# Optimization experiments

Measured on AMD Instinct MI355X. Metric: run time of the kernel, lower is better.

## Reference

```python
import jax, jax.numpy as jnp
import numpy as np

V, F, H, R = 10000, 768, 768, 49
B, T = 128, 32


def setup_inputs() -> dict:
    key = jax.random.key(0)
    ks = jax.random.split(key, 12)
    s = lambda *sh: 1.0 / np.sqrt(sh[-1])
    return {
        "features": jax.random.normal(ks[0], (B, R, F), jnp.float32),
        "captions": jax.random.randint(ks[1], (B, T), 0, V),
        "emb_W": jax.random.normal(ks[2], (V, H), jnp.float32),
        "attn_W": jax.random.normal(ks[3], (H, F + H), jnp.float32) * s(H, F + H),
        "attn_b": jnp.zeros((H,), jnp.float32),
        "attnv_W": jax.random.normal(ks[4], (1, H), jnp.float32) * s(1, H),
        "attnv_b": jnp.zeros((1,), jnp.float32),
        "W_ih": jax.random.normal(ks[5], (4 * H, H + F), jnp.float32) * s(1, H),
        "W_hh": jax.random.normal(ks[6], (4 * H, H), jnp.float32) * s(1, H),
        "b_ih": jnp.zeros((4 * H,), jnp.float32),
        "b_hh": jnp.zeros((4 * H,), jnp.float32),
        "fc_W": jax.random.normal(ks[7], (V, H), jnp.float32) * s(V, H),
        "fc_b": jnp.zeros((V,), jnp.float32),
    }


def reference(features, captions, emb_W, attn_W, attn_b, attnv_W, attnv_b,
              W_ih, W_hh, b_ih, b_hh, fc_W, fc_b):
    # initial hidden state (hidden_state=None branch)
    h0 = jnp.tanh(features.mean(axis=1))           # [B,H]
    c0 = jnp.zeros_like(h0)                        # [B,H]
    emb = emb_W[captions]                          # [B,T,H]

    # split attn_linear weight into feature/hidden parts; feature projection is
    # time-invariant so compute once outside the scan.
    Wf, Wh = attn_W[:, :F], attn_W[:, F:]
    feat_proj = jnp.einsum('brf,hf->brh', features, Wf)   # [B,R,H]
    v = attnv_W[0]                                 # [H]
    bias = b_ih + b_hh                             # [4H]

    def step(carry, emb_t):
        h, c = carry
        attn_hidden = jnp.tanh(feat_proj + (h @ Wh.T)[:, None, :] + attn_b)  # [B,R,H]
        scores = attn_hidden @ v + attnv_b[0]      # [B,R]
        alpha = jax.nn.softmax(scores, axis=1)
        context = jnp.einsum('br,brf->bf', alpha, features)  # [B,F]
        x = jnp.concatenate([emb_t, context], axis=1)        # [B,H+F]
        gates = x @ W_ih.T + h @ W_hh.T + bias     # [B,4H]
        i, f, g, o = jnp.split(gates, 4, axis=1)
        c_new = jax.nn.sigmoid(f) * c + jax.nn.sigmoid(i) * jnp.tanh(g)
        h_new = jax.nn.sigmoid(o) * jnp.tanh(c_new)
        out_t = h_new @ fc_W.T + fc_b              # [B,V] (dropout = identity, eval)
        return (h_new, c_new), out_t

    (h, c), outs = jax.lax.scan(step, (h0, c0), jnp.swapaxes(emb, 0, 1))
    outputs = jnp.swapaxes(outs, 0, 1)             # [B,T,V]
    return outputs, (h, c)
```

## Files before the change

### kernel.cpp

```cpp
#include <hip/hip_runtime.h>


typedef _Float16 f16x8 __attribute__((ext_vector_type(8)));
typedef _Float16 f16x4 __attribute__((ext_vector_type(4)));
typedef float f32x4 __attribute__((ext_vector_type(4)));

#define NB 128
#define NT 32
#define NV 10000
#define NH 768
#define NR 49
#define OUT_ELEMS 40960000

__device__ __forceinline__ float fast_tanh(float x) {
  x = fminf(9.f, fmaxf(-9.f, x));
  float e = __expf(2.f * x);
  return (e - 1.f) / (e + 1.f);
}
__device__ __forceinline__ float sigm(float x) { return 1.f / (1.f + __expf(-x)); }

__device__ __forceinline__ void gld16(const void* g, void* l) {
  __builtin_amdgcn_global_load_lds((const __attribute__((address_space(1))) void*)g,
                                   (__attribute__((address_space(3))) void*)l, 16, 0, 0);
}

template <int BM, int BN, int EPI>
__global__ __launch_bounds__(256) void gemm_f16(
    const _Float16* __restrict__ A, int lda,
    const _Float16* __restrict__ Bt, int ldb,
    void* __restrict__ Cv, const float* __restrict__ bias,
    int M, int N, int ksteps, int ksplit) {
  constexpr int BK = 64;
  __shared__ __attribute__((aligned(16))) _Float16 sAB[(BM + BN) * BK];
  _Float16* sA = sAB;
  _Float16* sB = sAB + BM * BK;
  const int tid = threadIdx.x;
  const int m0 = blockIdx.x * BM, n0 = blockIdx.y * BN;
  const int z = blockIdx.z;
  A += (size_t)z * ksplit;
  Bt += (size_t)z * ksplit;

  constexpr int WM = BM / 2, WN = BN / 2;
  constexpr int MF = WM / 16, NF = WN / 16;
  const int wid = tid >> 6, lane = tid & 63;
  const int wr = wid >> 1, wc = wid & 1;
  const int lr = lane & 15;
  const int lk = (lane >> 4) * 8;

  f32x4 acc[MF][NF] = {};

  for (int kt = 0; kt < ksteps; ++kt) {
    const int kbase = kt * BK;
#pragma unroll
    for (int i = 0; i < BM / 32; i++) {
      int idx = tid + i * 256;
      int row = idx >> 3, seg = idx & 7;
      gld16(A + (size_t)(m0 + row) * lda + kbase + seg * 8, sA + idx * 8);
    }
#pragma unroll
    for (int i = 0; i < BN / 32; i++) {
      int idx = tid + i * 256;
      int row = idx >> 3, seg = idx & 7;
      gld16(Bt + (size_t)(n0 + row) * ldb + kbase + seg * 8, sB + idx * 8);
    }
    __syncthreads();
#pragma unroll
    for (int kk = 0; kk < 2; ++kk) {
      f16x8 af[MF], bf[NF];
#pragma unroll
      for (int m = 0; m < MF; m++)
        af[m] = *(const f16x8*)&sA[(wr * WM + m * 16 + lr) * BK + kk * 32 + lk];
#pragma unroll
      for (int n = 0; n < NF; n++)
        bf[n] = *(const f16x8*)&sB[(wc * WN + n * 16 + lr) * BK + kk * 32 + lk];
#pragma unroll
      for (int m = 0; m < MF; m++)
#pragma unroll
        for (int n = 0; n < NF; n++)
          acc[m][n] = __builtin_amdgcn_mfma_f32_16x16x32_f16(af[m], bf[n], acc[m][n], 0, 0, 0);
    }
    __syncthreads();
  }

  const int rowb = (lane >> 4) * 4;
#pragma unroll
  for (int m = 0; m < MF; m++) {
    int gm = m0 + wr * WM + m * 16 + rowb;
#pragma unroll
    for (int n = 0; n < NF; n++) {
      int gn = n0 + wc * WN + n * 16 + lr;
#pragma unroll
      for (int j = 0; j < 4; j++) {
        int r = gm + j;
        if (EPI == 1) {
          float* C = (float*)Cv + (size_t)z * M * N;
          C[(size_t)r * N + gn] = acc[m][n][j];
        } else if (EPI == 3) {
          ((_Float16*)Cv)[(size_t)r * N + gn] = (_Float16)(acc[m][n][j] + bias[gn]);
        } else {
          ((_Float16*)Cv)[(size_t)r * N + gn] = (_Float16)acc[m][n][j];
        }
      }
    }
  }
}

__global__ __launch_bounds__(512) void gemm_fc(
    const _Float16* __restrict__ A, const _Float16* __restrict__ Bt,
    float* __restrict__ out, const float* __restrict__ bias, int N) {
  constexpr int BK = 64;
  __shared__ __attribute__((aligned(16))) _Float16 sAB[256 * BK];
  _Float16* sA = sAB;
  _Float16* sB = sAB + 128 * BK;
  const int tid = threadIdx.x;
  const int m0 = blockIdx.x * 128, n0 = blockIdx.y * 128;
  const int wid = tid >> 6, lane = tid & 63;
  const int wr = wid >> 1;
  const int wc = wid & 1;
  const int lr = lane & 15;
  const int lk = (lane >> 4) * 8;

  f32x4 acc[2][4] = {};

  for (int kt = 0; kt < 12; ++kt) {
    const int kbase = kt * BK;
#pragma unroll
    for (int i = 0; i < 2; i++) {
      int idx = tid + i * 512;
      int row = idx >> 3, seg = idx & 7;
      gld16(A + (size_t)(m0 + row) * NH + kbase + seg * 8, sA + idx * 8);
      int gr = n0 + row;
      if (gr >= N) gr = N - 1;
      gld16(Bt + (size_t)gr * NH + kbase + seg * 8, sB + idx * 8);
    }
    __syncthreads();
#pragma unroll
    for (int kk = 0; kk < 2; ++kk) {
      f16x8 af[2], bf[4];
#pragma unroll
      for (int m = 0; m < 2; m++)
        af[m] = *(const f16x8*)&sA[(wr * 32 + m * 16 + lr) * BK + kk * 32 + lk];
#pragma unroll
      for (int n = 0; n < 4; n++)
        bf[n] = *(const f16x8*)&sB[(wc * 64 + n * 16 + lr) * BK + kk * 32 + lk];
#pragma unroll
      for (int m = 0; m < 2; m++)
#pragma unroll
        for (int n = 0; n < 4; n++)
          acc[m][n] = __builtin_amdgcn_mfma_f32_16x16x32_f16(af[m], bf[n], acc[m][n], 0, 0, 0);
    }
    __syncthreads();
  }

  const int rowb = (lane >> 4) * 4;
  float* sC = (float*)sAB;
#pragma unroll
  for (int h = 0; h < 2; h++) {
    if ((wr >> 1) == h) {
#pragma unroll
      for (int m = 0; m < 2; m++)
#pragma unroll
        for (int n = 0; n < 4; n++)
#pragma unroll
          for (int j = 0; j < 4; j++)
            sC[((wr & 1) * 32 + m * 16 + rowb + j) * 128 + wc * 64 + n * 16 + lr] =
                acc[m][n][j];
    }
    __syncthreads();
#pragma unroll
    for (int i = 0; i < 4; i++) {
      int lrow = (tid >> 5) + i * 16;
      int col = (tid & 31) * 4;
      int gn = n0 + col;
      if (gn < N) {
        int r = m0 + h * 64 + lrow;
        int tt = r >> 7, b = r & 127;
        f32x4 val = *(f32x4*)&sC[lrow * 128 + col];
        f32x4 bb = *(const f32x4*)&bias[gn];
        val += bb;
        *(f32x4*)&out[((size_t)(b * NT + tt)) * NV + gn] = val;
      }
    }
    __syncthreads();
  }
}

__global__ __launch_bounds__(256) void k_scores(
    const _Float16* __restrict__ fp, const float* __restrict__ g1,
    const float* __restrict__ v, float* __restrict__ sc) {
  int wid = threadIdx.x >> 6, lane = threadIdx.x & 63;
  int p = blockIdx.x * 4 + wid;
  int b = p / NR;
  const _Float16* fpr = fp + (size_t)p * NH;
  const float* hw0 = g1 + (size_t)b * 3840;
  const float* hw1 = g1 + (size_t)NB * 3840 + (size_t)b * 3840;
  float s = 0.f;
#pragma unroll
  for (int it = 0; it < 3; it++) {
    int h = it * 256 + lane * 4;
    f16x4 fv = *(const f16x4*)(fpr + h);
    f32x4 a0 = *(const f32x4*)(hw0 + h);
    f32x4 a1 = *(const f32x4*)(hw1 + h);
    f32x4 vv = *(const f32x4*)(v + h);
#pragma unroll
    for (int j = 0; j < 4; j++) s += fast_tanh((float)fv[j] + a0[j] + a1[j]) * vv[j];
  }
#pragma unroll
  for (int off = 32; off; off >>= 1) s += __shfl_down(s, off);
  if (lane == 0) sc[p] = s;
}

__global__ __launch_bounds__(256) void k_ctx(const float* __restrict__ sc,
                                             const _Float16* __restrict__ feat16,
                                             _Float16* __restrict__ ctx16) {
  __shared__ float al[64];
  int b = blockIdx.x, tid = threadIdx.x;
  if (tid < 64) {
    float s = (tid < NR) ? sc[b * NR + tid] : -1e30f;
    float m = s;
#pragma unroll
    for (int off = 32; off; off >>= 1) m = fmaxf(m, __shfl_xor(m, off));
    float e = (tid < NR) ? __expf(s - m) : 0.f;
    float su = e;
#pragma unroll
    for (int off = 32; off; off >>= 1) su += __shfl_xor(su, off);
    al[tid] = e / su;
  }
  __syncthreads();
  int f = blockIdx.y * 256 + tid;
  const _Float16* fb = feat16 + (size_t)b * NR * NH + f;
  float acc = 0.f;
#pragma unroll
  for (int r = 0; r < NR; r++) acc += al[r] * (float)fb[(size_t)r * NH];
  ctx16[(size_t)b * NH + f] = (_Float16)acc;
}

__global__ void k_lstm2(const _Float16* __restrict__ ge_t, const float* __restrict__ g1,
                        const float* __restrict__ g2, const float* __restrict__ b_ih,
                        const float* __restrict__ b_hh, float* __restrict__ h,
                        float* __restrict__ c, _Float16* __restrict__ h16,
                        _Float16* __restrict__ Hall_t) {
  int b = blockIdx.x;
  int hh = blockIdx.y * 256 + threadIdx.x;
  const _Float16* ge = ge_t + (size_t)b * 3072;
  const float* a0 = g1 + (size_t)b * 3840 + 768;
  const float* a1 = g1 + (size_t)NB * 3840 + (size_t)b * 3840 + 768;
  const float* c0 = g2 + (size_t)b * 3072;
  const float* c1 = g2 + (size_t)NB * 3072 + (size_t)b * 3072;
  float gi = (float)ge[hh] + a0[hh] + a1[hh] + c0[hh] + c1[hh] + b_ih[hh] + b_hh[hh];
  float gf = (float)ge[768 + hh] + a0[768 + hh] + a1[768 + hh] + c0[768 + hh] + c1[768 + hh] +
             b_ih[768 + hh] + b_hh[768 + hh];
  float gg = (float)ge[1536 + hh] + a0[1536 + hh] + a1[1536 + hh] + c0[1536 + hh] +
             c1[1536 + hh] + b_ih[1536 + hh] + b_hh[1536 + hh];
  float go = (float)ge[2304 + hh] + a0[2304 + hh] + a1[2304 + hh] + c0[2304 + hh] +
             c1[2304 + hh] + b_ih[2304 + hh] + b_hh[2304 + hh];
  float i_ = sigm(gi), f_ = sigm(gf), g_ = fast_tanh(gg), o_ = sigm(go);
  float cn = f_ * c[b * NH + hh] + i_ * g_;
  float hn = o_ * fast_tanh(cn);
  c[b * NH + hh] = cn;
  h[b * NH + hh] = hn;
  h16[(size_t)b * NH + hh] = (_Float16)hn;
  Hall_t[(size_t)b * NH + hh] = (_Float16)hn;
}

__global__ void k_prep(const float* __restrict__ features, const float* __restrict__ attn_W,
                       const float* __restrict__ W_ih, const float* __restrict__ W_hh,
                       const int* __restrict__ captions, const float* __restrict__ emb_W,
                       _Float16* __restrict__ feat16, _Float16* __restrict__ Wf16,
                       _Float16* __restrict__ W1, _Float16* __restrict__ We,
                       _Float16* __restrict__ Wc, _Float16* __restrict__ emb16,
                       float* __restrict__ h, float* __restrict__ c,
                       _Float16* __restrict__ h16) {
  const int blk = blockIdx.x, tid = threadIdx.x;
  if (blk < 18816) {
    int i = blk * 256 + tid;
    feat16[i] = (_Float16)features[i];
  } else if (blk < 21120) {
    int q = (blk - 18816) * 256 + tid;
    int j = q / NH, k = q - j * NH;
    Wf16[q] = (_Float16)attn_W[(size_t)j * 1536 + k];
  } else if (blk < 32640) {
    int q = (blk - 21120) * 256 + tid;
    int j = q / NH, k = q - j * NH;
    W1[q] = (_Float16)(j < NH ? attn_W[(size_t)j * 1536 + 768 + k]
                              : W_hh[(size_t)(j - NH) * NH + k]);
  } else if (blk < 41856) {
    int q = (blk - 32640) * 256 + tid;
    int j = q / NH, k = q - j * NH;
    We[q] = (_Float16)W_ih[(size_t)j * 1536 + k];
  } else if (blk < 51072) {
    int q = (blk - 41856) * 256 + tid;
    int j = q / NH, k = q - j * NH;
    Wc[q] = (_Float16)W_ih[(size_t)j * 1536 + 768 + k];
  } else if (blk < 63360) {
    int q = (blk - 51072) * 256 + tid;
    int row = q / NH, k = q - row * NH;
    int t = row >> 7, b = row & 127;
    int tok = captions[b * NT + t];
    emb16[q] = (_Float16)emb_W[(size_t)tok * NH + k];
  } else {
    int q = blk - 63360;
    int b = q / 3;
    int f = (q - b * 3) * 256 + tid;
    float s = 0.f;
#pragma unroll 7
    for (int r = 0; r < NR; r++) s += features[((size_t)(b * NR + r)) * NH + f];
    float h0 = tanhf(s * (1.f / 49.f));
    h[b * NH + f] = h0;
    c[b * NH + f] = 0.f;
    h16[(size_t)b * NH + f] = (_Float16)h0;
  }
}

__global__ void k_f32_to_f16(const float* __restrict__ src, _Float16* __restrict__ dst, int n) {
  int i = blockIdx.x * 256 + threadIdx.x;
  if (i < n) dst[i] = (_Float16)src[i];
}

__global__ void k_tail(const float* __restrict__ h, const float* __restrict__ c,
                       float* __restrict__ out) {
  int i = blockIdx.x * 256 + threadIdx.x;
  out[OUT_ELEMS + i] = h[i];
  out[OUT_ELEMS + NB * NH + i] = c[i];
}

extern "C" void kernel_launch(void* const* d_in, const int* in_sizes, int n_in,
                              void* d_out, int out_size, void* d_ws, size_t ws_size,
                              hipStream_t stream) {
  const float* features = (const float*)d_in[0];
  const int* captions = (const int*)d_in[1];
  const float* emb_W = (const float*)d_in[2];
  const float* attn_W = (const float*)d_in[3];
  const float* attn_b = (const float*)d_in[4];
  const float* attnv_W = (const float*)d_in[5];
  const float* W_ih = (const float*)d_in[7];
  const float* W_hh = (const float*)d_in[8];
  const float* b_ih = (const float*)d_in[9];
  const float* b_hh = (const float*)d_in[10];
  const float* fc_W = (const float*)d_in[11];
  const float* fc_b = (const float*)d_in[12];
  float* out = (float*)d_out;

  char* p = (char*)d_ws;
  _Float16* Gemb16 = (_Float16*)p;  p += 25165824;
  _Float16* fcW16 = Gemb16;
  _Float16* emb16 = (_Float16*)p;   p += 6291456;
  _Float16* feat16 = (_Float16*)p;  p += 9633792;
  _Float16* fp16 = (_Float16*)p;    p += 9633792;
  _Float16* Wf16 = (_Float16*)p;    p += 1179648;
  _Float16* W1 = (_Float16*)p;      p += 5898240;
  _Float16* We16 = (_Float16*)p;    p += 4718592;
  _Float16* Wc16 = (_Float16*)p;    p += 4718592;
  _Float16* H_all = (_Float16*)p;   p += 6291456;
  float* g1 = (float*)p;            p += 3932160;
  float* g2 = (float*)p;            p += 3145728;
  float* scores = (float*)p;        p += 25088;
  _Float16* ctx16 = (_Float16*)p;   p += 196608;
  _Float16* h16 = (_Float16*)p;     p += 196608;
  float* hbuf = (float*)p;          p += 393216;
  float* cbuf = (float*)p;          p += 393216;

  k_prep<<<dim3(63744), 256, 0, stream>>>(features, attn_W, W_ih, W_hh, captions, emb_W,
                                          feat16, Wf16, W1, We16, Wc16, emb16,
                                          hbuf, cbuf, h16);
  gemm_f16<128, 128, 3><<<dim3(49, 6, 1), 256, 0, stream>>>(
      feat16, 768, Wf16, 768, fp16, attn_b, 6272, 768, 12, 0);
  gemm_f16<128, 128, 4><<<dim3(32, 24, 1), 256, 0, stream>>>(
      emb16, 768, We16, 768, Gemb16, nullptr, 4096, 3072, 12, 0);

  for (int t = 0; t < NT; t++) {
    if (t > 0)
      k_lstm2<<<dim3(128, 3), 256, 0, stream>>>(
          Gemb16 + (size_t)(t - 1) * NB * 3072, g1, g2, b_ih, b_hh, hbuf, cbuf, h16,
          H_all + (size_t)(t - 1) * NB * NH);
    gemm_f16<64, 64, 1><<<dim3(2, 60, 2), 256, 0, stream>>>(
        h16, 768, W1, 768, g1, nullptr, 128, 3840, 6, 384);
    k_scores<<<dim3(1568), 256, 0, stream>>>(fp16, g1, attnv_W, scores);
    k_ctx<<<dim3(128, 3), 256, 0, stream>>>(scores, feat16, ctx16);
    gemm_f16<64, 64, 1><<<dim3(2, 48, 2), 256, 0, stream>>>(
        ctx16, 768, Wc16, 768, g2, nullptr, 128, 3072, 6, 384);
  }
  k_lstm2<<<dim3(128, 3), 256, 0, stream>>>(
      Gemb16 + (size_t)(NT - 1) * NB * 3072, g1, g2, b_ih, b_hh, hbuf, cbuf, h16,
      H_all + (size_t)(NT - 1) * NB * NH);

  k_f32_to_f16<<<dim3(30000), 256, 0, stream>>>(fc_W, fcW16, 7680000);
  gemm_fc<<<dim3(32, 79), 512, 0, stream>>>(H_all, fcW16, out, fc_b, NV);
  k_tail<<<dim3(384), 256, 0, stream>>>(hbuf, cbuf, out);
}
```

Baseline: 1.111 ms.

## Shrink critical-path GEMM per step and move W_hh product off it

The per-step hidden projection GEMM now covers only the attention part (Wh, 768 columns) with a 3-way K split, so k_scores waits on a smaller GEMM. The W_hh gate product moves into the context GEMM launch as extra z-slices (4-way partial buffers), and k_lstm2 sums four partials. The two setup GEMMs are merged into one launch, and gemm_fc switches to 256 threads with larger per-warp tiles. The trade-off is more partial-sum traffic in lstm and fewer waves in gemm_fc.

```diff
diff --git a/kernel.cpp b/kernel.cpp
--- a/kernel.cpp
+++ b/kernel.cpp
@@ -24,59 +24,114 @@
                                    (__attribute__((address_space(3))) void*)l, 16, 0, 0);
 }
 
-template <int BM, int BN, int EPI>
-__global__ __launch_bounds__(256) void gemm_f16(
-    const _Float16* __restrict__ A, int lda,
-    const _Float16* __restrict__ Bt, int ldb,
-    void* __restrict__ Cv, const float* __restrict__ bias,
-    int M, int N, int ksteps, int ksplit) {
+template <int KSTEPS, int KSPLIT>
+__global__ __launch_bounds__(256) void gemm64(
+    const _Float16* __restrict__ A, const _Float16* __restrict__ Bt,
+    float* __restrict__ C, int N) {
   constexpr int BK = 64;
-  __shared__ __attribute__((aligned(16))) _Float16 sAB[(BM + BN) * BK];
+  __shared__ __attribute__((aligned(16))) _Float16 sAB[128 * BK];
   _Float16* sA = sAB;
-  _Float16* sB = sAB + BM * BK;
+  _Float16* sB = sAB + 64 * BK;
   const int tid = threadIdx.x;
-  const int m0 = blockIdx.x * BM, n0 = blockIdx.y * BN;
+  const int m0 = blockIdx.x * 64, n0 = blockIdx.y * 64;
   const int z = blockIdx.z;
-  A += (size_t)z * ksplit;
-  Bt += (size_t)z * ksplit;
-
-  constexpr int WM = BM / 2, WN = BN / 2;
-  constexpr int MF = WM / 16, NF = WN / 16;
+  A += (size_t)z * KSPLIT;
+  Bt += (size_t)z * KSPLIT;
+  C += (size_t)z * 128 * N;
+
   const int wid = tid >> 6, lane = tid & 63;
   const int wr = wid >> 1, wc = wid & 1;
-  const int lr = lane & 15;
-  const int lk = (lane >> 4) * 8;
-
-  f32x4 acc[MF][NF] = {};
-
-  for (int kt = 0; kt < ksteps; ++kt) {
+  const int lr = lane & 15, lk = (lane >> 4) * 8;
+
+  f32x4 acc[2][2] = {};
+
+  for (int kt = 0; kt < KSTEPS; ++kt) {
     const int kbase = kt * BK;
 #pragma unroll
-    for (int i = 0; i < BM / 32; i++) {
+    for (int i = 0; i < 2; i++) {
       int idx = tid + i * 256;
       int row = idx >> 3, seg = idx & 7;
-      gld16(A + (size_t)(m0 + row) * lda + kbase + seg * 8, sA + idx * 8);
-    }
-#pragma unroll
-    for (int i = 0; i < BN / 32; i++) {
+      gld16(A + (size_t)(m0 + row) * NH + kbase + seg * 8, sA + idx * 8);
+      gld16(Bt + (size_t)(n0 + row) * NH + kbase + seg * 8, sB + idx * 8);
+    }
+    __syncthreads();
+#pragma unroll
+    for (int kk = 0; kk < 2; ++kk) {
+      f16x8 af[2], bf[2];
+#pragma unroll
+      for (int m = 0; m < 2; m++)
+        af[m] = *(const f16x8*)&sA[(wr * 32 + m * 16 + lr) * BK + kk * 32 + lk];
+#pragma unroll
+      for (int n = 0; n < 2; n++)
+        bf[n] = *(const f16x8*)&sB[(wc * 32 + n * 16 + lr) * BK + kk * 32 + lk];
+#pragma unroll
+      for (int m = 0; m < 2; m++)
+#pragma unroll
+        for (int n = 0; n < 2; n++)
+          acc[m][n] = __builtin_amdgcn_mfma_f32_16x16x32_f16(af[m], bf[n], acc[m][n], 0, 0, 0);
+    }
+    __syncthreads();
+  }
+
+  const int rowb = (lane >> 4) * 4;
+#pragma unroll
+  for (int m = 0; m < 2; m++) {
+    int gm = m0 + wr * 32 + m * 16 + rowb;
+#pragma unroll
+    for (int n = 0; n < 2; n++) {
+      int gn = n0 + wc * 32 + n * 16 + lr;
+#pragma unroll
+      for (int j = 0; j < 4; j++) C[(size_t)(gm + j) * N + gn] = acc[m][n][j];
+    }
+  }
+}
+
+__global__ __launch_bounds__(256) void gemm_g2m(
+    const _Float16* __restrict__ ctx16, const _Float16* __restrict__ Wc,
+    const _Float16* __restrict__ h16, const _Float16* __restrict__ Whh,
+    float* __restrict__ C) {
+  constexpr int BK = 64;
+  __shared__ __attribute__((aligned(16))) _Float16 sAB[128 * BK];
+  _Float16* sA = sAB;
+  _Float16* sB = sAB + 64 * BK;
+  const int tid = threadIdx.x;
+  const int m0 = blockIdx.x * 64, n0 = blockIdx.y * 64;
+  const int z = blockIdx.z;
+  const _Float16* A = (z >> 1) ? h16 : ctx16;
+  const _Float16* Bt = (z >> 1) ? Whh : Wc;
+  A += (size_t)(z & 1) * 384;
+  Bt += (size_t)(z & 1) * 384;
+  C += (size_t)z * 128 * 3072;
+
+  const int wid = tid >> 6, lane = tid & 63;
+  const int wr = wid >> 1, wc = wid & 1;
+  const int lr = lane & 15, lk = (lane >> 4) * 8;
+
+  f32x4 acc[2][2] = {};
+
+  for (int kt = 0; kt < 6; ++kt) {
+    const int kbase = kt * BK;
+#pragma unroll
+    for (int i = 0; i < 2; i++) {
       int idx = tid + i * 256;
       int row = idx >> 3, seg = idx & 7;
-      gld16(Bt + (size_t)(n0 + row) * ldb + kbase + seg * 8, sB + idx * 8);
+      gld16(A + (size_t)(m0 + row) * NH + kbase + seg * 8, sA + idx * 8);
+      gld16(Bt + (size_t)(n0 + row) * NH + kbase + seg * 8, sB + idx * 8);
     }
     __syncthreads();
 #pragma unroll
     for (int kk = 0; kk < 2; ++kk) {
-      f16x8 af[MF], bf[NF];
-#pragma unroll
-      for (int m = 0; m < MF; m++)
-        af[m] = *(const f16x8*)&sA[(wr * WM + m * 16 + lr) * BK + kk * 32 + lk];
-#pragma unroll
-      for (int n = 0; n < NF; n++)
-        bf[n] = *(const f16x8*)&sB[(wc * WN + n * 16 + lr) * BK + kk * 32 + lk];
-#pragma unroll
-      for (int m = 0; m < MF; m++)
-#pragma unroll
-        for (int n = 0; n < NF; n++)
+      f16x8 af[2], bf[2];
+#pragma unroll
+      for (int m = 0; m < 2; m++)
+        af[m] = *(const f16x8*)&sA[(wr * 32 + m * 16 + lr) * BK + kk * 32 + lk];
+#pragma unroll
+      for (int n = 0; n < 2; n++)
+        bf[n] = *(const f16x8*)&sB[(wc * 32 + n * 16 + lr) * BK + kk * 32 + lk];
+#pragma unroll
+      for (int m = 0; m < 2; m++)
+#pragma unroll
+        for (int n = 0; n < 2; n++)
           acc[m][n] = __builtin_amdgcn_mfma_f32_16x16x32_f16(af[m], bf[n], acc[m][n], 0, 0, 0);
     }
     __syncthreads();
@@ -84,28 +139,87 @@
 
   const int rowb = (lane >> 4) * 4;
 #pragma unroll
-  for (int m = 0; m < MF; m++) {
-    int gm = m0 + wr * WM + m * 16 + rowb;
-#pragma unroll
-    for (int n = 0; n < NF; n++) {
-      int gn = n0 + wc * WN + n * 16 + lr;
+  for (int m = 0; m < 2; m++) {
+    int gm = m0 + wr * 32 + m * 16 + rowb;
+#pragma unroll
+    for (int n = 0; n < 2; n++) {
+      int gn = n0 + wc * 32 + n * 16 + lr;
+#pragma unroll
+      for (int j = 0; j < 4; j++) C[(size_t)(gm + j) * 3072 + gn] = acc[m][n][j];
+    }
+  }
+}
+
+__global__ __launch_bounds__(256) void gemm_phA(
+    const _Float16* __restrict__ feat16, const _Float16* __restrict__ Wf16,
+    const float* __restrict__ attn_b, _Float16* __restrict__ fp16,
+    const _Float16* __restrict__ emb16, const _Float16* __restrict__ We16,
+    _Float16* __restrict__ Gemb16) {
+  constexpr int BK = 64;
+  __shared__ __attribute__((aligned(16))) _Float16 sAB[256 * BK];
+  _Float16* sA = sAB;
+  _Float16* sB = sAB + 128 * BK;
+  const int blk = blockIdx.x, tid = threadIdx.x;
+  const bool isFP = blk < 294;
+  const int bx = isFP ? (blk % 49) : ((blk - 294) % 32);
+  const int by = isFP ? (blk / 49) : ((blk - 294) / 32);
+  const _Float16* A = isFP ? feat16 : emb16;
+  const _Float16* Bt = isFP ? Wf16 : We16;
+  const int m0 = bx * 128, n0 = by * 128;
+
+  const int wid = tid >> 6, lane = tid & 63;
+  const int wr = wid >> 1, wc = wid & 1;
+  const int lr = lane & 15, lk = (lane >> 4) * 8;
+
+  f32x4 acc[4][4] = {};
+
+  for (int kt = 0; kt < 12; ++kt) {
+    const int kbase = kt * BK;
+#pragma unroll
+    for (int i = 0; i < 4; i++) {
+      int idx = tid + i * 256;
+      int row = idx >> 3, seg = idx & 7;
+      gld16(A + (size_t)(m0 + row) * NH + kbase + seg * 8, sA + idx * 8);
+      gld16(Bt + (size_t)(n0 + row) * NH + kbase + seg * 8, sB + idx * 8);
+    }
+    __syncthreads();
+#pragma unroll
+    for (int kk = 0; kk < 2; ++kk) {
+      f16x8 af[4], bf[4];
+#pragma unroll
+      for (int m = 0; m < 4; m++)
+        af[m] = *(const f16x8*)&sA[(wr * 64 + m * 16 + lr) * BK + kk * 32 + lk];
+#pragma unroll
+      for (int n = 0; n < 4; n++)
+        bf[n] = *(const f16x8*)&sB[(wc * 64 + n * 16 + lr) * BK + kk * 32 + lk];
+#pragma unroll
+      for (int m = 0; m < 4; m++)
+#pragma unroll
+        for (int n = 0; n < 4; n++)
+          acc[m][n] = __builtin_amdgcn_mfma_f32_16x16x32_f16(af[m], bf[n], acc[m][n], 0, 0, 0);
+    }
+    __syncthreads();
+  }
+
+  const int rowb = (lane >> 4) * 4;
+#pragma unroll
+  for (int m = 0; m < 4; m++) {
+    int gm = m0 + wr * 64 + m * 16 + rowb;
+#pragma unroll
+    for (int n = 0; n < 4; n++) {
+      int gn = n0 + wc * 64 + n * 16 + lr;
 #pragma unroll
       for (int j = 0; j < 4; j++) {
-        int r = gm + j;
-        if (EPI == 1) {
-          float* C = (float*)Cv + (size_t)z * M * N;
-          C[(size_t)r * N + gn] = acc[m][n][j];
-        } else if (EPI == 3) {
-          ((_Float16*)Cv)[(size_t)r * N + gn] = (_Float16)(acc[m][n][j] + bias[gn]);
-        } else {
-          ((_Float16*)Cv)[(size_t)r * N + gn] = (_Float16)acc[m][n][j];
-        }
+        if (isFP)
+          fp16[(size_t)(gm + j) * NH + gn] = (_Float16)(acc[m][n][j] + attn_b[gn]);
+        else
+          Gemb16[(size_t)(gm + j) * 3072 + gn] = (_Float16)acc[m][n][j];
       }
     }
   }
 }
 
-__global__ __launch_bounds__(512) void gemm_fc(
+__global__ __launch_bounds__(256) void gemm_fc(
     const _Float16* __restrict__ A, const _Float16* __restrict__ Bt,
     float* __restrict__ out, const float* __restrict__ bias, int N) {
   constexpr int BK = 64;
@@ -115,18 +229,16 @@
   const int tid = threadIdx.x;
   const int m0 = blockIdx.x * 128, n0 = blockIdx.y * 128;
   const int wid = tid >> 6, lane = tid & 63;
-  const int wr = wid >> 1;
-  const int wc = wid & 1;
-  const int lr = lane & 15;
-  const int lk = (lane >> 4) * 8;
-
-  f32x4 acc[2][4] = {};
+  const int wr = wid >> 1, wc = wid & 1;
+  const int lr = lane & 15, lk = (lane >> 4) * 8;
+
+  f32x4 acc[4][4] = {};
 
   for (int kt = 0; kt < 12; ++kt) {
     const int kbase = kt * BK;
 #pragma unroll
-    for (int i = 0; i < 2; i++) {
-      int idx = tid + i * 512;
+    for (int i = 0; i < 4; i++) {
+      int idx = tid + i * 256;
       int row = idx >> 3, seg = idx & 7;
       gld16(A + (size_t)(m0 + row) * NH + kbase + seg * 8, sA + idx * 8);
       int gr = n0 + row;
@@ -136,15 +248,15 @@
     __syncthreads();
 #pragma unroll
     for (int kk = 0; kk < 2; ++kk) {
-      f16x8 af[2], bf[4];
-#pragma unroll
-      for (int m = 0; m < 2; m++)
-        af[m] = *(const f16x8*)&sA[(wr * 32 + m * 16 + lr) * BK + kk * 32 + lk];
+      f16x8 af[4], bf[4];
+#pragma unroll
+      for (int m = 0; m < 4; m++)
+        af[m] = *(const f16x8*)&sA[(wr * 64 + m * 16 + lr) * BK + kk * 32 + lk];
 #pragma unroll
       for (int n = 0; n < 4; n++)
         bf[n] = *(const f16x8*)&sB[(wc * 64 + n * 16 + lr) * BK + kk * 32 + lk];
 #pragma unroll
-      for (int m = 0; m < 2; m++)
+      for (int m = 0; m < 4; m++)
 #pragma unroll
         for (int n = 0; n < 4; n++)
           acc[m][n] = __builtin_amdgcn_mfma_f32_16x16x32_f16(af[m], bf[n], acc[m][n], 0, 0, 0);
@@ -156,20 +268,19 @@
   float* sC = (float*)sAB;
 #pragma unroll
   for (int h = 0; h < 2; h++) {
-    if ((wr >> 1) == h) {
-#pragma unroll
-      for (int m = 0; m < 2; m++)
+    if (wr == h) {
+#pragma unroll
+      for (int m = 0; m < 4; m++)
 #pragma unroll
         for (int n = 0; n < 4; n++)
 #pragma unroll
           for (int j = 0; j < 4; j++)
-            sC[((wr & 1) * 32 + m * 16 + rowb + j) * 128 + wc * 64 + n * 16 + lr] =
-                acc[m][n][j];
-    }
-    __syncthreads();
-#pragma unroll
-    for (int i = 0; i < 4; i++) {
-      int lrow = (tid >> 5) + i * 16;
+            sC[(m * 16 + rowb + j) * 128 + wc * 64 + n * 16 + lr] = acc[m][n][j];
+    }
+    __syncthreads();
+#pragma unroll
+    for (int i = 0; i < 8; i++) {
+      int lrow = (tid >> 5) + i * 8;
       int col = (tid & 31) * 4;
       int gn = n0 + col;
       if (gn < N) {
@@ -186,14 +297,15 @@
 }
 
 __global__ __launch_bounds__(256) void k_scores(
-    const _Float16* __restrict__ fp, const float* __restrict__ g1,
+    const _Float16* __restrict__ fp, const float* __restrict__ g1a,
     const float* __restrict__ v, float* __restrict__ sc) {
   int wid = threadIdx.x >> 6, lane = threadIdx.x & 63;
   int p = blockIdx.x * 4 + wid;
   int b = p / NR;
   const _Float16* fpr = fp + (size_t)p * NH;
-  const float* hw0 = g1 + (size_t)b * 3840;
-  const float* hw1 = g1 + (size_t)NB * 3840 + (size_t)b * 3840;
+  const float* hw0 = g1a + (size_t)b * NH;
+  const float* hw1 = g1a + (size_t)NB * NH + (size_t)b * NH;
+  const float* hw2 = g1a + (size_t)2 * NB * NH + (size_t)b * NH;
   float s = 0.f;
 #pragma unroll
   for (int it = 0; it < 3; it++) {
@@ -201,9 +313,10 @@
     f16x4 fv = *(const f16x4*)(fpr + h);
     f32x4 a0 = *(const f32x4*)(hw0 + h);
     f32x4 a1 = *(const f32x4*)(hw1 + h);
+    f32x4 a2 = *(const f32x4*)(hw2 + h);
     f32x4 vv = *(const f32x4*)(v + h);
 #pragma unroll
-    for (int j = 0; j < 4; j++) s += fast_tanh((float)fv[j] + a0[j] + a1[j]) * vv[j];
+    for (int j = 0; j < 4; j++) s += fast_tanh((float)fv[j] + a0[j] + a1[j] + a2[j]) * vv[j];
   }
 #pragma unroll
   for (int off = 32; off; off >>= 1) s += __shfl_down(s, off);
@@ -235,25 +348,24 @@
   ctx16[(size_t)b * NH + f] = (_Float16)acc;
 }
 
-__global__ void k_lstm2(const _Float16* __restrict__ ge_t, const float* __restrict__ g1,
-                        const float* __restrict__ g2, const float* __restrict__ b_ih,
-                        const float* __restrict__ b_hh, float* __restrict__ h,
-                        float* __restrict__ c, _Float16* __restrict__ h16,
-                        _Float16* __restrict__ Hall_t) {
+__global__ void k_lstm2(const _Float16* __restrict__ ge_t, const float* __restrict__ gbuf,
+                        const float* __restrict__ b_ih, const float* __restrict__ b_hh,
+                        float* __restrict__ h, float* __restrict__ c,
+                        _Float16* __restrict__ h16, _Float16* __restrict__ Hall_t) {
   int b = blockIdx.x;
   int hh = blockIdx.y * 256 + threadIdx.x;
   const _Float16* ge = ge_t + (size_t)b * 3072;
-  const float* a0 = g1 + (size_t)b * 3840 + 768;
-  const float* a1 = g1 + (size_t)NB * 3840 + (size_t)b * 3840 + 768;
-  const float* c0 = g2 + (size_t)b * 3072;
-  const float* c1 = g2 + (size_t)NB * 3072 + (size_t)b * 3072;
-  float gi = (float)ge[hh] + a0[hh] + a1[hh] + c0[hh] + c1[hh] + b_ih[hh] + b_hh[hh];
-  float gf = (float)ge[768 + hh] + a0[768 + hh] + a1[768 + hh] + c0[768 + hh] + c1[768 + hh] +
+  const float* p0 = gbuf + (size_t)b * 3072;
+  const float* p1 = p0 + (size_t)NB * 3072;
+  const float* p2 = p1 + (size_t)NB * 3072;
+  const float* p3 = p2 + (size_t)NB * 3072;
+  float gi = (float)ge[hh] + p0[hh] + p1[hh] + p2[hh] + p3[hh] + b_ih[hh] + b_hh[hh];
+  float gf = (float)ge[768 + hh] + p0[768 + hh] + p1[768 + hh] + p2[768 + hh] + p3[768 + hh] +
              b_ih[768 + hh] + b_hh[768 + hh];
-  float gg = (float)ge[1536 + hh] + a0[1536 + hh] + a1[1536 + hh] + c0[1536 + hh] +
-             c1[1536 + hh] + b_ih[1536 + hh] + b_hh[1536 + hh];
-  float go = (float)ge[2304 + hh] + a0[2304 + hh] + a1[2304 + hh] + c0[2304 + hh] +
-             c1[2304 + hh] + b_ih[2304 + hh] + b_hh[2304 + hh];
+  float gg = (float)ge[1536 + hh] + p0[1536 + hh] + p1[1536 + hh] + p2[1536 + hh] +
+             p3[1536 + hh] + b_ih[1536 + hh] + b_hh[1536 + hh];
+  float go = (float)ge[2304 + hh] + p0[2304 + hh] + p1[2304 + hh] + p2[2304 + hh] +
+             p3[2304 + hh] + b_ih[2304 + hh] + b_hh[2304 + hh];
   float i_ = sigm(gi), f_ = sigm(gf), g_ = fast_tanh(gg), o_ = sigm(go);
   float cn = f_ * c[b * NH + hh] + i_ * g_;
   float hn = o_ * fast_tanh(cn);
@@ -267,10 +379,10 @@
                        const float* __restrict__ W_ih, const float* __restrict__ W_hh,
                        const int* __restrict__ captions, const float* __restrict__ emb_W,
                        _Float16* __restrict__ feat16, _Float16* __restrict__ Wf16,
-                       _Float16* __restrict__ W1, _Float16* __restrict__ We,
-                       _Float16* __restrict__ Wc, _Float16* __restrict__ emb16,
-                       float* __restrict__ h, float* __restrict__ c,
-                       _Float16* __restrict__ h16) {
+                       _Float16* __restrict__ Wh16, _Float16* __restrict__ Whh16,
+                       _Float16* __restrict__ We, _Float16* __restrict__ Wc,
+                       _Float16* __restrict__ emb16, float* __restrict__ h,
+                       float* __restrict__ c, _Float16* __restrict__ h16) {
   const int blk = blockIdx.x, tid = threadIdx.x;
   if (blk < 18816) {
     int i = blk * 256 + tid;
@@ -279,11 +391,13 @@
     int q = (blk - 18816) * 256 + tid;
     int j = q / NH, k = q - j * NH;
     Wf16[q] = (_Float16)attn_W[(size_t)j * 1536 + k];
-  } else if (blk < 32640) {
+  } else if (blk < 23424) {
     int q = (blk - 21120) * 256 + tid;
     int j = q / NH, k = q - j * NH;
-    W1[q] = (_Float16)(j < NH ? attn_W[(size_t)j * 1536 + 768 + k]
-                              : W_hh[(size_t)(j - NH) * NH + k]);
+    Wh16[q] = (_Float16)attn_W[(size_t)j * 1536 + 768 + k];
+  } else if (blk < 32640) {
+    int q = (blk - 23424) * 256 + tid;
+    Whh16[q] = (_Float16)W_hh[q];
   } else if (blk < 41856) {
     int q = (blk - 32640) * 256 + tid;
     int j = q / NH, k = q - j * NH;
@@ -348,12 +462,13 @@
   _Float16* feat16 = (_Float16*)p;  p += 9633792;
   _Float16* fp16 = (_Float16*)p;    p += 9633792;
   _Float16* Wf16 = (_Float16*)p;    p += 1179648;
-  _Float16* W1 = (_Float16*)p;      p += 5898240;
+  _Float16* Wh16 = (_Float16*)p;    p += 1179648;
+  _Float16* Whh16 = (_Float16*)p;   p += 4718592;
   _Float16* We16 = (_Float16*)p;    p += 4718592;
   _Float16* Wc16 = (_Float16*)p;    p += 4718592;
   _Float16* H_all = (_Float16*)p;   p += 6291456;
-  float* g1 = (float*)p;            p += 3932160;
-  float* g2 = (float*)p;            p += 3145728;
+  float* g1a = (float*)p;           p += 1179648;
+  float* gbuf = (float*)p;          p += 6291456;
   float* scores = (float*)p;        p += 25088;
   _Float16* ctx16 = (_Float16*)p;   p += 196608;
   _Float16* h16 = (_Float16*)p;     p += 196608;
@@ -361,30 +476,25 @@
   float* cbuf = (float*)p;          p += 393216;
 
   k_prep<<<dim3(63744), 256, 0, stream>>>(features, attn_W, W_ih, W_hh, captions, emb_W,
-                                          feat16, Wf16, W1, We16, Wc16, emb16,
+                                          feat16, Wf16, Wh16, Whh16, We16, Wc16, emb16,
                                           hbuf, cbuf, h16);
-  gemm_f16<128, 128, 3><<<dim3(49, 6, 1), 256, 0, stream>>>(
-      feat16, 768, Wf16, 768, fp16, attn_b, 6272, 768, 12, 0);
-  gemm_f16<128, 128, 4><<<dim3(32, 24, 1), 256, 0, stream>>>(
-      emb16, 768, We16, 768, Gemb16, nullptr, 4096, 3072, 12, 0);
+  gemm_phA<<<dim3(1062), 256, 0, stream>>>(feat16, Wf16, attn_b, fp16, emb16, We16, Gemb16);
 
   for (int t = 0; t < NT; t++) {
     if (t > 0)
       k_lstm2<<<dim3(128, 3), 256, 0, stream>>>(
-          Gemb16 + (size_t)(t - 1) * NB * 3072, g1, g2, b_ih, b_hh, hbuf, cbuf, h16,
+          Gemb16 + (size_t)(t - 1) * NB * 3072, gbuf, b_ih, b_hh, hbuf, cbuf, h16,
           H_all + (size_t)(t - 1) * NB * NH);
-    gemm_f16<64, 64, 1><<<dim3(2, 60, 2), 256, 0, stream>>>(
-        h16, 768, W1, 768, g1, nullptr, 128, 3840, 6, 384);
-    k_scores<<<dim3(1568), 256, 0, stream>>>(fp16, g1, attnv_W, scores);
+    gemm64<4, 256><<<dim3(2, 12, 3), 256, 0, stream>>>(h16, Wh16, g1a, NH);
+    k_scores<<<dim3(1568), 256, 0, stream>>>(fp16, g1a, attnv_W, scores);
     k_ctx<<<dim3(128, 3), 256, 0, stream>>>(scores, feat16, ctx16);
-    gemm_f16<64, 64, 1><<<dim3(2, 48, 2), 256, 0, stream>>>(
-        ctx16, 768, Wc16, 768, g2, nullptr, 128, 3072, 6, 384);
+    gemm_g2m<<<dim3(2, 48, 4), 256, 0, stream>>>(ctx16, Wc16, h16, Whh16, gbuf);
   }
   k_lstm2<<<dim3(128, 3), 256, 0, stream>>>(
-      Gemb16 + (size_t)(NT - 1) * NB * 3072, g1, g2, b_ih, b_hh, hbuf, cbuf, h16,
+      Gemb16 + (size_t)(NT - 1) * NB * 3072, gbuf, b_ih, b_hh, hbuf, cbuf, h16,
       H_all + (size_t)(NT - 1) * NB * NH);
 
   k_f32_to_f16<<<dim3(30000), 256, 0, stream>>>(fc_W, fcW16, 7680000);
-  gemm_fc<<<dim3(32, 79), 512, 0, stream>>>(H_all, fcW16, out, fc_b, NV);
+  gemm_fc<<<dim3(32, 79), 256, 0, stream>>>(H_all, fcW16, out, fc_b, NV);
   k_tail<<<dim3(384), 256, 0, stream>>>(hbuf, cbuf, out);
 }
```

Result: faster. 1.023 ms (-8.0%).
